# Optimization experiments

Measured on AMD Instinct MI355X. Metric: run time of the kernel, lower is better.

## Reference

```python
import jax, jax.numpy as jnp
import numpy as np

U_N, I_N, D, L, R = 50000, 25000, 64, 2, 2
E_UI, E_TR, E_II = 500000, 600000, 400000
B, K = 512, 100
EPS = 1e-8
LAMB = 0.5
L2_NORM = 1e-4


def setup_inputs() -> dict:
    key = jax.random.key(0)
    ks = jax.random.split(key, 16)
    f = lambda k, s: jax.random.normal(k, s, dtype=jnp.float32) * 0.05
    ri = lambda k, s, lo, hi: jax.random.randint(k, s, lo, hi, dtype=jnp.int32)
    return {
        "user_embedding": f(ks[0], (U_N, D)),
        "item_embedding": f(ks[1], (I_N, D)),
        "user_item_W": f(ks[2], (L, D, D)),
        "item_item_W": f(ks[3], (R, L, D, D)),
        "behavior_W": f(ks[4], (R, D * (L + 1), D * (L + 1))),
        "mgnn_weight": jax.random.normal(ks[5], (R,), dtype=jnp.float32),
        "rel_rows": ri(ks[6], (R, E_UI), 0, U_N),
        "rel_cols": ri(ks[7], (R, E_UI), 0, I_N),
        "train_rows": ri(ks[8], (E_TR,), 0, U_N),
        "train_cols": ri(ks[9], (E_TR,), 0, I_N),
        "ig_rows": ri(ks[10], (R, E_II), 0, I_N),
        "ig_cols": ri(ks[11], (R, E_II), 0, I_N),
        "user_behavior_degree": ri(ks[12], (U_N, R), 1, 50),
        "item_graph_degree": ri(ks[13], (R, I_N), 1, 50),
        "users": ri(ks[14], (B,), 0, U_N),
        "items": ri(ks[15], (B, K), 0, I_N),
    }


def _seg(data, seg_ids, n):
    return jax.ops.segment_sum(data, seg_ids, num_segments=n)


def _propagate(ue, ie, W_ui, W_ii, mgnn_weight,
               rel_rows, rel_cols, train_rows, train_cols,
               ig_rows, ig_cols, ubd, igd):
    Un, In = ue.shape[0], ie.shape[0]
    ubd_f = ubd.astype(jnp.float32)
    igd_f = igd.astype(jnp.float32)
    # per-user behavior mixing weights alpha_{u,t}
    w = jax.nn.softmax(mgnn_weight)                       # [R]
    total = ubd_f @ w[:, None]                            # [U,1]
    ubw = ubd_f * w[None, :] / (total + EPS)              # [U,R]
    # item degree from train matrix column sums (unit values)
    item_deg = _seg(jnp.ones((train_cols.shape[0],), jnp.float32), train_cols, In)[:, None] + EPS
    U_cur, I_cur = ue, ie
    U_list, I_list = [ue], [ie]
    S_lists = [[ie] for _ in range(R)]
    for l in range(L):
        # user <- item aggregation per behavior, weighted sum over behaviors
        U_neighbor = jnp.zeros_like(U_cur)
        for r in range(R):
            p = _seg(I_cur[rel_cols[r]], rel_rows[r], Un) / (ubd_f[:, r:r + 1] + EPS)
            U_neighbor = U_neighbor + ubw[:, r:r + 1] * p
        U_new = U_neighbor @ W_ui[l]
        # item <- user aggregation through train matrix transpose
        I_user = _seg(U_cur[train_rows], train_cols, In) / item_deg
        I_new = I_user @ W_ui[l]
        # item-item propagation per behavior
        for r in range(R):
            agg = _seg(I_cur[ig_cols[r]], ig_rows[r], In) / (igd_f[r][:, None] + EPS)
            S_lists[r].append(agg @ W_ii[r, l])
        U_cur, I_cur = U_new, I_new
        U_list.append(U_cur)
        I_list.append(I_cur)
    U_final = jnp.concatenate(U_list, axis=1)             # [U, D*(L+1)]
    I_final = jnp.concatenate(I_list, axis=1)             # [I, D*(L+1)]
    S_final = [jnp.concatenate(s, axis=1) for s in S_lists]
    return U_final, I_final, S_final


def reference(user_embedding, item_embedding, user_item_W, item_item_W,
              behavior_W, mgnn_weight, rel_rows, rel_cols, train_rows,
              train_cols, ig_rows, ig_cols, user_behavior_degree,
              item_graph_degree, users, items):
    Uf, If, Sf = _propagate(user_embedding, item_embedding, user_item_W,
                            item_item_W, mgnn_weight, rel_rows, rel_cols,
                            train_rows, train_cols, ig_rows, ig_cols,
                            user_behavior_degree, item_graph_degree)
    bu = Uf[users]                                        # [B, dt]
    bi = If[items]                                        # [B, K, dt]
    score1 = jnp.einsum('bd,bkd->bk', bu, bi)
    ubd_f = user_behavior_degree.astype(jnp.float32)
    Un = user_embedding.shape[0]
    score2 = jnp.zeros_like(score1)
    for r in range(R):
        s_emb = Sf[r]
        agg = _seg(s_emb[rel_cols[r]], rel_rows[r], Un) / (ubd_f[:, r:r + 1] + EPS)
        user_proj = agg @ behavior_W[r]                   # [U, dt]
        item_proj = s_emb @ behavior_W[r]                 # [I, dt]
        # gather-then-dot instead of full [B,I] matmul + gather (same math)
        score2 = score2 + jnp.einsum('bd,bkd->bk', user_proj[users], item_proj[items])
    score2 = score2 / R
    scores = LAMB * score1 + (1.0 - LAMB) * score2
    n_cand = items.shape[1]
    # original squares the [B,K,dt]-expanded user emb, hence the *K factor
    L2_loss = L2_NORM * (jnp.sum(bu ** 2) * n_cand + jnp.sum(bi ** 2))
    return scores, L2_loss
```

## Files before the change

kernel.cpp:

```cpp
#include <hip/hip_runtime.h>
#include <hip/hip_bf16.h>

#define U_NN   50000
#define I_NN   25000
#define DIM    64
#define EUI    500000
#define ETR    600000
#define EII    400000
#define NB     512
#define NK     100
#define EPSF   1e-8f
#define LAMBF  0.5f
#define L2NF   1e-4f
#define S_UI   48
#define S_TR   64
#define S_IG   48

typedef unsigned short bfu;

__device__ __forceinline__ bfu f2bf(float f) {
  unsigned int u = __float_as_uint(f);
  return (bfu)((u + 0x7fffu + ((u >> 16) & 1u)) >> 16);
}

__device__ __forceinline__ float4 bf4(uint2 p) {
  float4 r;
  r.x = __uint_as_float(p.x << 16);
  r.y = __uint_as_float(p.x & 0xffff0000u);
  r.z = __uint_as_float(p.y << 16);
  r.w = __uint_as_float(p.y & 0xffff0000u);
  return r;
}


__global__ void k_prep_user(const int* __restrict__ ubd, const float* __restrict__ mg,
                            float* __restrict__ scale1, float* __restrict__ scale2) {
  int u = blockIdx.x * 256 + threadIdx.x;
  if (u >= U_NN) return;
  float m0 = mg[0], m1 = mg[1];
  float mx = fmaxf(m0, m1);
  float e0 = expf(m0 - mx), e1 = expf(m1 - mx);
  float inv = 1.0f / (e0 + e1);
  float w0 = e0 * inv, w1 = e1 * inv;
  float d0 = (float)ubd[u * 2 + 0], d1 = (float)ubd[u * 2 + 1];
  float total = d0 * w0 + d1 * w1;
  float it = 1.0f / (total + EPSF);
  scale1[u * 2 + 0] = (d0 * w0 * it) / (d0 + EPSF);
  scale1[u * 2 + 1] = (d1 * w1 * it) / (d1 + EPSF);
  scale2[u * 2 + 0] = 1.0f / (d0 + EPSF);
  scale2[u * 2 + 1] = 1.0f / (d1 + EPSF);
}

__global__ void k_inv_int(const int* __restrict__ d, float* __restrict__ o, int n) {
  int i = blockIdx.x * 256 + threadIdx.x;
  if (i >= n) return;
  o[i] = 1.0f / ((float)d[i] + EPSF);
}

__global__ void k_transpose192(const float* __restrict__ BW, float* __restrict__ BWT) {
  int r = blockIdx.y;
  int i = blockIdx.x * 256 + threadIdx.x;
  if (i >= 192 * 192) return;
  int row = i / 192, col = i - row * 192;
  BWT[(size_t)r * 36864 + row * 192 + col] = BW[(size_t)r * 36864 + col * 192 + row];
}

__global__ void k_cvt(const float* __restrict__ s, bfu* __restrict__ d, int n4) {
  int i = blockIdx.x * 256 + threadIdx.x;
  if (i >= n4) return;
  float4 v = reinterpret_cast<const float4*>(s)[i];
  ushort4 o;
  o.x = f2bf(v.x); o.y = f2bf(v.y); o.z = f2bf(v.z); o.w = f2bf(v.w);
  reinterpret_cast<ushort4*>(d)[i] = o;
}


struct FillDesc { const int* key; const int* val; int n; int* cur; int* ec; int stride; int nk; };
struct FillDescs { FillDesc d[5]; };

__global__ void k_fill_r(FillDescs ds, int pass) {
  FillDesc sd = ds.d[blockIdx.y];
  int qk = sd.nk >> 2;
  int klo = qk * pass;
  int khi = (pass == 3) ? sd.nk : klo + qk;
  int base = blockIdx.x * 2048 + threadIdx.x;
  int kk[8], pp[8];
#pragma unroll
  for (int i = 0; i < 8; i++) {
    int e = base + i * 256;
    kk[i] = -1;
    if (e < sd.n) { int k = sd.key[e]; if (k >= klo && k < khi) kk[i] = k; }
  }
#pragma unroll
  for (int i = 0; i < 8; i++)
    pp[i] = (kk[i] >= 0) ? atomicAdd(&sd.cur[kk[i]], 1) : 0;
#pragma unroll
  for (int i = 0; i < 8; i++)
    if (kk[i] >= 0 && pp[i] < sd.stride)
      sd.ec[(size_t)kk[i] * sd.stride + pp[i]] = sd.val[base + i * 256];
}

struct AggDesc {
  const int* ecA; const int* curA; int strideA;
  const int* ecB; const int* curB; int strideB;
  const bfu* src;
  const float* W;
  float* out;
  bfu* outb;
  const float* sc;
  const int* map;
  int n;
  int mode;
};
struct AggDescs { AggDesc d[4]; };

__device__ __forceinline__ float4 wred(float4 a) {
  a.x += __shfl_xor(a.x, 16, 64); a.y += __shfl_xor(a.y, 16, 64);
  a.z += __shfl_xor(a.z, 16, 64); a.w += __shfl_xor(a.w, 16, 64);
  a.x += __shfl_xor(a.x, 32, 64); a.y += __shfl_xor(a.y, 32, 64);
  a.z += __shfl_xor(a.z, 32, 64); a.w += __shfl_xor(a.w, 32, 64);
  return a;
}

__device__ __forceinline__ float rdlane(float v, int l) {
  return __uint_as_float(__builtin_amdgcn_readlane(__float_as_uint(v), l));
}

#define ACC4(A, v) { A.x += v.x; A.y += v.y; A.z += v.z; A.w += v.w; }

__device__ __forceinline__ void gather4b(const int* __restrict__ l0, int d0,
                                         const int* __restrict__ l1, int d1,
                                         const int* __restrict__ l2, int d2,
                                         const int* __restrict__ l3, int d3,
                                         const bfu* __restrict__ src, int c4, int sub,
                                         float4& A0, float4& A1, float4& A2, float4& A3) {
  int j0 = sub, j1 = sub, j2 = sub, j3 = sub;
  while (j0 < d0 && j1 < d1 && j2 < d2 && j3 < d3) {
    uint2 p0 = *reinterpret_cast<const uint2*>(src + (size_t)l0[j0] * DIM + c4);
    uint2 p1 = *reinterpret_cast<const uint2*>(src + (size_t)l1[j1] * DIM + c4);
    uint2 p2 = *reinterpret_cast<const uint2*>(src + (size_t)l2[j2] * DIM + c4);
    uint2 p3 = *reinterpret_cast<const uint2*>(src + (size_t)l3[j3] * DIM + c4);
    float4 v0 = bf4(p0), v1 = bf4(p1), v2 = bf4(p2), v3 = bf4(p3);
    ACC4(A0, v0); ACC4(A1, v1); ACC4(A2, v2); ACC4(A3, v3);
    j0 += 4; j1 += 4; j2 += 4; j3 += 4;
  }
  for (; j0 < d0; j0 += 4) { float4 v = bf4(*reinterpret_cast<const uint2*>(src + (size_t)l0[j0] * DIM + c4)); ACC4(A0, v); }
  for (; j1 < d1; j1 += 4) { float4 v = bf4(*reinterpret_cast<const uint2*>(src + (size_t)l1[j1] * DIM + c4)); ACC4(A1, v); }
  for (; j2 < d2; j2 += 4) { float4 v = bf4(*reinterpret_cast<const uint2*>(src + (size_t)l2[j2] * DIM + c4)); ACC4(A2, v); }
  for (; j3 < d3; j3 += 4) { float4 v = bf4(*reinterpret_cast<const uint2*>(src + (size_t)l3[j3] * DIM + c4)); ACC4(A3, v); }
}

__device__ __forceinline__ void mm2(const float* wreg, float4 x0, float4 x1,
                                    float& y0, float& y1) {
  y0 = 0.f; y1 = 0.f;
#pragma unroll
  for (int sl = 0; sl < 16; sl++) {
    y0 = fmaf(rdlane(x0.x, sl), wreg[4 * sl + 0], y0);
    y0 = fmaf(rdlane(x0.y, sl), wreg[4 * sl + 1], y0);
    y0 = fmaf(rdlane(x0.z, sl), wreg[4 * sl + 2], y0);
    y0 = fmaf(rdlane(x0.w, sl), wreg[4 * sl + 3], y0);
    y1 = fmaf(rdlane(x1.x, sl), wreg[4 * sl + 0], y1);
    y1 = fmaf(rdlane(x1.y, sl), wreg[4 * sl + 1], y1);
    y1 = fmaf(rdlane(x1.z, sl), wreg[4 * sl + 2], y1);
    y1 = fmaf(rdlane(x1.w, sl), wreg[4 * sl + 3], y1);
  }
}

__device__ __forceinline__ float4 scale4(float4 a, float s) {
  float4 r; r.x = a.x * s; r.y = a.y * s; r.z = a.z * s; r.w = a.w * s; return r;
}

__global__ __launch_bounds__(256) void k_agg_mm(AggDescs ds) {
  AggDesc sd = ds.d[blockIdx.y];
  int rowBlk = blockIdx.x * 16;
  if (rowBlk >= sd.n) return;
  int t = threadIdx.x;
  int wv = t >> 6, lane = t & 63;
  int sub = lane >> 4, c4 = (lane & 15) * 4;
  float wreg[64];
#pragma unroll
  for (int k = 0; k < 64; k++) wreg[k] = sd.W[k * 64 + lane];
  int rowBase = rowBlk + wv * 4;

  if (sd.mode == 0) {
    for (int rep = 0; rep < 2; rep++) {
      int row0 = rowBase + rep * 2;
      int row1 = row0 + 1;
      if (row0 >= sd.n) break;
      bool ok1 = row1 < sd.n;
      int u0 = sd.map ? sd.map[row0] : row0;
      int u1 = ok1 ? (sd.map ? sd.map[row1] : row1) : u0;
      int dA0 = sd.curA[u0], dB0 = sd.curB[u0];
      int dA1 = ok1 ? sd.curA[u1] : 0;
      int dB1 = ok1 ? sd.curB[u1] : 0;
      const int* lA0 = sd.ecA + (size_t)u0 * sd.strideA;
      const int* lB0 = sd.ecB + (size_t)u0 * sd.strideB;
      const int* lA1 = sd.ecA + (size_t)u1 * sd.strideA;
      const int* lB1 = sd.ecB + (size_t)u1 * sd.strideB;
      float4 aA0 = {0,0,0,0}, aB0 = {0,0,0,0}, aA1 = {0,0,0,0}, aB1 = {0,0,0,0};
      gather4b(lA0, dA0, lB0, dB0, lA1, dA1, lB1, dB1, sd.src, c4, sub,
               aA0, aB0, aA1, aB1);
      aA0 = wred(aA0); aB0 = wred(aB0); aA1 = wred(aA1); aB1 = wred(aB1);
      float sA0 = sd.sc[u0 * 2], sB0 = sd.sc[u0 * 2 + 1];
      float sA1 = sd.sc[u1 * 2], sB1 = sd.sc[u1 * 2 + 1];
      float4 x0, x1;
      x0.x = sA0 * aA0.x + sB0 * aB0.x; x0.y = sA0 * aA0.y + sB0 * aB0.y;
      x0.z = sA0 * aA0.z + sB0 * aB0.z; x0.w = sA0 * aA0.w + sB0 * aB0.w;
      x1.x = sA1 * aA1.x + sB1 * aB1.x; x1.y = sA1 * aA1.y + sB1 * aB1.y;
      x1.z = sA1 * aA1.z + sB1 * aB1.z; x1.w = sA1 * aA1.w + sB1 * aB1.w;
      float y0, y1;
      mm2(wreg, x0, x1, y0, y1);
      sd.out[(size_t)row0 * DIM + lane] = y0;
      if (sd.outb) sd.outb[(size_t)row0 * DIM + lane] = f2bf(y0);
      if (ok1) {
        sd.out[(size_t)row1 * DIM + lane] = y1;
        if (sd.outb) sd.outb[(size_t)row1 * DIM + lane] = f2bf(y1);
      }
    }
  } else {
    int row0 = rowBase, row1 = rowBase + 1, row2 = rowBase + 2, row3 = rowBase + 3;
    if (row0 >= sd.n) return;
    bool ok1 = row1 < sd.n, ok2 = row2 < sd.n, ok3 = row3 < sd.n;
    int u1c = ok1 ? row1 : row0, u2c = ok2 ? row2 : row0, u3c = ok3 ? row3 : row0;
    int d0 = sd.curA[row0];
    int d1 = ok1 ? sd.curA[row1] : 0;
    int d2 = ok2 ? sd.curA[row2] : 0;
    int d3 = ok3 ? sd.curA[row3] : 0;
    const int* l0 = sd.ecA + (size_t)row0 * sd.strideA;
    const int* l1 = sd.ecA + (size_t)u1c * sd.strideA;
    const int* l2 = sd.ecA + (size_t)u2c * sd.strideA;
    const int* l3 = sd.ecA + (size_t)u3c * sd.strideA;
    float4 a0 = {0,0,0,0}, a1 = {0,0,0,0}, a2 = {0,0,0,0}, a3 = {0,0,0,0};
    gather4b(l0, d0, l1, d1, l2, d2, l3, d3, sd.src, c4, sub, a0, a1, a2, a3);
    a0 = wred(a0); a1 = wred(a1); a2 = wred(a2); a3 = wred(a3);
    float s0, s1, s2, s3;
    if (sd.mode == 1) {
      s0 = 1.0f / ((float)d0 + EPSF); s1 = 1.0f / ((float)d1 + EPSF);
      s2 = 1.0f / ((float)d2 + EPSF); s3 = 1.0f / ((float)d3 + EPSF);
    } else {
      s0 = sd.sc[row0]; s1 = ok1 ? sd.sc[row1] : 0.f;
      s2 = ok2 ? sd.sc[row2] : 0.f; s3 = ok3 ? sd.sc[row3] : 0.f;
    }
    float4 x0 = scale4(a0, s0), x1 = scale4(a1, s1);
    float4 x2 = scale4(a2, s2), x3 = scale4(a3, s3);
    float y0, y1, y2, y3;
    mm2(wreg, x0, x1, y0, y1);
    mm2(wreg, x2, x3, y2, y3);
    sd.out[(size_t)row0 * DIM + lane] = y0;
    if (sd.outb) sd.outb[(size_t)row0 * DIM + lane] = f2bf(y0);
    if (ok1) { sd.out[(size_t)row1 * DIM + lane] = y1;
               if (sd.outb) sd.outb[(size_t)row1 * DIM + lane] = f2bf(y1); }
    if (ok2) { sd.out[(size_t)row2 * DIM + lane] = y2;
               if (sd.outb) sd.outb[(size_t)row2 * DIM + lane] = f2bf(y2); }
    if (ok3) { sd.out[(size_t)row3 * DIM + lane] = y3;
               if (sd.outb) sd.outb[(size_t)row3 * DIM + lane] = f2bf(y3); }
  }
}

__global__ void k_agg_score(const int* __restrict__ ec0, const int* __restrict__ cur0,
                            const int* __restrict__ ec1, const int* __restrict__ cur1,
                            const int* __restrict__ users, const float* __restrict__ scale2,
                            const bfu* __restrict__ I0b,
                            const bfu* __restrict__ S0ab, const bfu* __restrict__ S0bb,
                            const bfu* __restrict__ S1ab, const bfu* __restrict__ S1bb,
                            float* __restrict__ aggB) {
  int b = blockIdx.x, r = blockIdx.y;
  int w = threadIdx.x >> 6, lane = threadIdx.x & 63;
  int sub = lane >> 4, c4 = (lane & 15) * 4;
  int u = users[b];
  const int* ec = (r ? ec1 : ec0) + (size_t)u * S_UI;
  int d = (r ? cur1 : cur0)[u];
  const bfu* src = (w == 0) ? I0b : (w == 1) ? (r ? S1ab : S0ab) : (r ? S1bb : S0bb);
  float4 acc = {0.f, 0.f, 0.f, 0.f};
  for (int j = sub; j < d; j += 4) {
    float4 v = bf4(*reinterpret_cast<const uint2*>(src + (size_t)ec[j] * DIM + c4));
    acc.x += v.x; acc.y += v.y; acc.z += v.z; acc.w += v.w;
  }
  acc = wred(acc);
  if (sub == 0) {
    float s = scale2[u * 2 + r];
    float4 o = { acc.x * s, acc.y * s, acc.z * s, acc.w * s };
    *reinterpret_cast<float4*>(aggB + ((size_t)r * NB + b) * 192 + w * 64 + c4) = o;
  }
}


struct M192Desc { const float* X0; const float* X1; const float* X2; int xStride;
                  const float* W; float* Y; int n; };
struct M192Descs { M192Desc d[2]; };

__global__ void k_matmul192(M192Descs ds) {
  M192Desc sd = ds.d[blockIdx.y];
  int r0 = blockIdx.x * 64;
  if (r0 >= sd.n) return;
  __shared__ float Wl[32 * 192];
  __shared__ float xs[64][32];
  int t = threadIdx.x;
  int rg = t >> 6, col = t & 63;
  float acc[16][3];
#pragma unroll
  for (int j = 0; j < 16; j++) { acc[j][0] = 0.f; acc[j][1] = 0.f; acc[j][2] = 0.f; }
  for (int kc = 0; kc < 6; kc++) {
    const float* Xc = (kc < 2) ? sd.X0 : ((kc < 4) ? sd.X1 : sd.X2);
    int xoff = (kc & 1) * 32;
#pragma unroll
    for (int tt = 0; tt < 8; tt++) {
      int e = t + tt * 256;
      int rr = e >> 5, cc = e & 31;
      int row = r0 + rr;
      xs[rr][cc] = (row < sd.n) ? Xc[(size_t)row * sd.xStride + xoff + cc] : 0.0f;
    }
#pragma unroll
    for (int tt = 0; tt < 24; tt++) {
      int e = t + tt * 256;
      Wl[e] = sd.W[(size_t)(kc * 32) * 192 + e];
    }
    __syncthreads();
    for (int k = 0; k < 32; k++) {
      float w0 = Wl[k * 192 + col];
      float w1 = Wl[k * 192 + 64 + col];
      float w2 = Wl[k * 192 + 128 + col];
#pragma unroll
      for (int j = 0; j < 16; j++) {
        float x = xs[rg * 16 + j][k];
        acc[j][0] += x * w0; acc[j][1] += x * w1; acc[j][2] += x * w2;
      }
    }
    __syncthreads();
  }
  for (int j = 0; j < 16; j++) {
    int row = r0 + rg * 16 + j;
    if (row < sd.n) {
      sd.Y[(size_t)row * 192 + col]       = acc[j][0];
      sd.Y[(size_t)row * 192 + 64 + col]  = acc[j][1];
      sd.Y[(size_t)row * 192 + 128 + col] = acc[j][2];
    }
  }
}

__global__ void k_score_all(const int* __restrict__ users, const int* __restrict__ items,
                            const float* __restrict__ U0, const float* __restrict__ U1,
                            const float* __restrict__ U2B,
                            const float* __restrict__ I0, const float* __restrict__ I1,
                            const float* __restrict__ I2,
                            const float* __restrict__ S0a, const float* __restrict__ S0b,
                            const float* __restrict__ S1a, const float* __restrict__ S1b,
                            const float* __restrict__ upB2,
                            float* __restrict__ out) {
  int b = blockIdx.x, t = threadIdx.x;
  int wave = t >> 6, lane = t & 63;
  int u = users[b];
  float uf0 = U0[(size_t)u * 64 + lane];
  float uf1 = U1[(size_t)u * 64 + lane];
  float uf2 = U2B[(size_t)b * 64 + lane];
  const float* u20 = upB2 + (size_t)b * 192;
  const float* u21 = upB2 + (size_t)(NB + b) * 192;
  float av0 = u20[lane] + u21[lane];
  float a01 = u20[64 + lane], a02 = u20[128 + lane];
  float a11 = u21[64 + lane], a12 = u21[128 + lane];
  float l2acc = (wave == 0) ? (uf0 * uf0 + uf1 * uf1 + uf2 * uf2) * (float)NK : 0.0f;
  for (int k = wave * 25; k < wave * 25 + 25; k++) {
    int it = items[b * NK + k];
    float v0  = I0[(size_t)it * 64 + lane];
    float v1  = I1[(size_t)it * 64 + lane];
    float v2  = I2[(size_t)it * 64 + lane];
    float w0a = S0a[(size_t)it * 64 + lane];
    float w0b = S0b[(size_t)it * 64 + lane];
    float w1a = S1a[(size_t)it * 64 + lane];
    float w1b = S1b[(size_t)it * 64 + lane];
    float p = LAMBF * (uf0 * v0 + uf1 * v1 + uf2 * v2)
            + 0.25f * (av0 * v0 + a01 * w0a + a02 * w0b + a11 * w1a + a12 * w1b);
    l2acc += v0 * v0 + v1 * v1 + v2 * v2;
#pragma unroll
    for (int m = 1; m < 64; m <<= 1) p += __shfl_xor(p, m, 64);
    if (lane == 0) out[b * NK + k] = p;
  }
#pragma unroll
  for (int m = 1; m < 64; m <<= 1) l2acc += __shfl_xor(l2acc, m, 64);
  __shared__ float ws4[4];
  if (lane == 0) ws4[wave] = l2acc;
  __syncthreads();
  if (t == 0) atomicAdd(out + NB * NK, (ws4[0] + ws4[1] + ws4[2] + ws4[3]) * L2NF);
}


extern "C" void kernel_launch(void* const* d_in, const int* in_sizes, int n_in,
                              void* d_out, int out_size, void* d_ws, size_t ws_size,
                              hipStream_t stream) {
  const float* U0  = (const float*)d_in[0];
  const float* I0  = (const float*)d_in[1];
  const float* Wui = (const float*)d_in[2];
  const float* Wii = (const float*)d_in[3];
  const float* BW  = (const float*)d_in[4];
  const float* mg  = (const float*)d_in[5];
  const int* rel_rows   = (const int*)d_in[6];
  const int* rel_cols   = (const int*)d_in[7];
  const int* train_rows = (const int*)d_in[8];
  const int* train_cols = (const int*)d_in[9];
  const int* ig_rows    = (const int*)d_in[10];
  const int* ig_cols    = (const int*)d_in[11];
  const int* ubd        = (const int*)d_in[12];
  const int* igd        = (const int*)d_in[13];
  const int* users      = (const int*)d_in[14];
  const int* items      = (const int*)d_in[15];
  float* out = (float*)d_out;

  char* wptr = (char*)d_ws;
  auto alloci = [&](size_t n) -> int* {
    int* p = (int*)wptr;
    wptr += ((n * 4 + 255) / 256) * 256;
    return p;
  };
  auto allocf = [&](size_t n) -> float* { return (float*)alloci(n); };
  auto allocb = [&](size_t n) -> bfu* {
    bfu* p = (bfu*)wptr;
    wptr += ((n * 2 + 255) / 256) * 256;
    return p;
  };

  float* scale1 = allocf((size_t)U_NN * 2);
  float* scale2 = allocf((size_t)U_NN * 2);
  float* invig  = allocf((size_t)2 * I_NN);
  float* BWT    = allocf((size_t)2 * 192 * 192);
  int* c0  = alloci(U_NN);
  int* c1  = alloci(U_NN);
  int* cT  = alloci(I_NN);
  int* cG0 = alloci(I_NN);
  int* cG1 = alloci(I_NN);
  size_t curBytes = (size_t)(wptr - (char*)c0);
  int* ec0  = alloci((size_t)U_NN * S_UI);
  int* ec1  = alloci((size_t)U_NN * S_UI);
  int* ecT  = alloci((size_t)I_NN * S_TR);
  int* ecG0 = alloci((size_t)I_NN * S_IG);
  int* ecG1 = alloci((size_t)I_NN * S_IG);
  float* U1  = allocf((size_t)U_NN * 64);
  float* I1  = allocf((size_t)I_NN * 64);
  float* I2  = allocf((size_t)I_NN * 64);
  float* S0a = allocf((size_t)I_NN * 64);
  float* S0b = allocf((size_t)I_NN * 64);
  float* S1a = allocf((size_t)I_NN * 64);
  float* S1b = allocf((size_t)I_NN * 64);
  float* U2B = allocf((size_t)NB * 64);
  float* aggB = allocf((size_t)2 * NB * 192);
  float* upBt = allocf((size_t)2 * NB * 192);
  float* upB2 = allocf((size_t)2 * NB * 192);
  bfu* U0b  = allocb((size_t)U_NN * 64);
  bfu* I0b  = allocb((size_t)I_NN * 64);
  bfu* U1b  = allocb((size_t)U_NN * 64);
  bfu* I1b  = allocb((size_t)I_NN * 64);
  bfu* S0ab = allocb((size_t)I_NN * 64);
  bfu* S0bb = allocb((size_t)I_NN * 64);
  bfu* S1ab = allocb((size_t)I_NN * 64);
  bfu* S1bb = allocb((size_t)I_NN * 64);

  const int gU = (U_NN + 255) / 256;
  const int gI2 = (2 * I_NN + 255) / 256;

  hipMemsetAsync(c0, 0, curBytes, stream);
  k_prep_user<<<gU, 256, 0, stream>>>(ubd, mg, scale1, scale2);
  k_inv_int<<<gI2, 256, 0, stream>>>(igd, invig, 2 * I_NN);
  k_transpose192<<<dim3(144, 2), 256, 0, stream>>>(BW, BWT);
  k_cvt<<<(U_NN * 16 + 255) / 256, 256, 0, stream>>>(U0, U0b, U_NN * 16);
  k_cvt<<<(I_NN * 16 + 255) / 256, 256, 0, stream>>>(I0, I0b, I_NN * 16);

  FillDescs fd;
  fd.d[0] = { rel_rows,       rel_cols,       EUI, c0,  ec0,  S_UI, U_NN };
  fd.d[1] = { rel_rows + EUI, rel_cols + EUI, EUI, c1,  ec1,  S_UI, U_NN };
  fd.d[2] = { train_cols,     train_rows,     ETR, cT,  ecT,  S_TR, I_NN };
  fd.d[3] = { ig_rows,        ig_cols,        EII, cG0, ecG0, S_IG, I_NN };
  fd.d[4] = { ig_rows + EII,  ig_cols + EII,  EII, cG1, ecG1, S_IG, I_NN };
  const int gE8 = (ETR + 2047) / 2048;
  for (int p = 0; p < 4; p++)
    k_fill_r<<<dim3(gE8, 5), 256, 0, stream>>>(fd, p);

  AggDescs a0;
  a0.d[0] = { ec0, c0, S_UI, ec1, c1, S_UI, I0b, Wui,            U1,  U1b,  scale1, nullptr, U_NN, 0 };
  a0.d[1] = { ecT, cT, S_TR, nullptr, nullptr, 0, U0b, Wui,      I1,  I1b,  nullptr, nullptr, I_NN, 1 };
  a0.d[2] = { ecG0, cG0, S_IG, nullptr, nullptr, 0, I0b, Wii + 0 * 4096, S0a, S0ab, invig,        nullptr, I_NN, 2 };
  a0.d[3] = { ecG1, cG1, S_IG, nullptr, nullptr, 0, I0b, Wii + 2 * 4096, S1a, S1ab, invig + I_NN, nullptr, I_NN, 2 };
  k_agg_mm<<<dim3((U_NN + 15) / 16, 4), 256, 0, stream>>>(a0);

  AggDescs a1;
  a1.d[0] = { ec0, c0, S_UI, ec1, c1, S_UI, I1b, Wui + 4096,     U2B, nullptr, scale1, users,  NB,   0 };
  a1.d[1] = { ecT, cT, S_TR, nullptr, nullptr, 0, U1b, Wui + 4096, I2, nullptr, nullptr, nullptr, I_NN, 1 };
  a1.d[2] = { ecG0, cG0, S_IG, nullptr, nullptr, 0, I1b, Wii + 1 * 4096, S0b, S0bb, invig,        nullptr, I_NN, 2 };
  a1.d[3] = { ecG1, cG1, S_IG, nullptr, nullptr, 0, I1b, Wii + 3 * 4096, S1b, S1bb, invig + I_NN, nullptr, I_NN, 2 };
  k_agg_mm<<<dim3((I_NN + 15) / 16, 4), 256, 0, stream>>>(a1);

  k_agg_score<<<dim3(NB, 2), 192, 0, stream>>>(ec0, c0, ec1, c1, users, scale2,
                                               I0b, S0ab, S0bb, S1ab, S1bb, aggB);
  M192Descs mU;
  mU.d[0] = { aggB,            aggB + 64,            aggB + 128,            192, BW,         upBt,            NB };
  mU.d[1] = { aggB + NB * 192, aggB + NB * 192 + 64, aggB + NB * 192 + 128, 192, BW + 36864, upBt + NB * 192, NB };
  k_matmul192<<<dim3((NB + 63) / 64, 2), 256, 0, stream>>>(mU);
  M192Descs mU2;
  mU2.d[0] = { upBt,            upBt + 64,            upBt + 128,            192, BWT,         upB2,            NB };
  mU2.d[1] = { upBt + NB * 192, upBt + NB * 192 + 64, upBt + NB * 192 + 128, 192, BWT + 36864, upB2 + NB * 192, NB };
  k_matmul192<<<dim3((NB + 63) / 64, 2), 256, 0, stream>>>(mU2);

  hipMemsetAsync(out + (size_t)NB * NK, 0, 4, stream);
  k_score_all<<<NB, 256, 0, stream>>>(users, items, U0, U1, U2B,
                                      I0, I1, I2, S0a, S0b, S1a, S1b, upB2, out);
}
```

Before: 619.3 us.

## Transform-then-aggregate: precompute X@W in bf16 before neighbor gather

Reorders each propagation layer so node features are first multiplied by the 64x64 weight in a separate dense kernel that writes bf16, then the gather-aggregate kernel only sums the pre-transformed rows and scales them. This relies on linearity, (sum x)W = sum(xW). It removes the readlane-based matmul and the 64-register weight load from the latency-bound gather kernel. The gather loop is also rewritten as predicated, max-degree-bounded iterations with two edges per step, and results are written as vectorized float4. In exchange it adds two extra kernel launches and extra memory traffic for eight transformed tables, and rounding now happens after the transform rather than before.

```diff
diff --git a/kernel.cpp b/kernel.cpp
--- a/kernel.cpp
+++ b/kernel.cpp
@@ -100,19 +100,6 @@
       sd.ec[(size_t)kk[i] * sd.stride + pp[i]] = sd.val[base + i * 256];
 }
 
-struct AggDesc {
-  const int* ecA; const int* curA; int strideA;
-  const int* ecB; const int* curB; int strideB;
-  const bfu* src;
-  const float* W;
-  float* out;
-  bfu* outb;
-  const float* sc;
-  const int* map;
-  int n;
-  int mode;
-};
-struct AggDescs { AggDesc d[4]; };
 
 __device__ __forceinline__ float4 wred(float4 a) {
   a.x += __shfl_xor(a.x, 16, 64); a.y += __shfl_xor(a.y, 16, 64);
@@ -126,28 +113,20 @@
   return __uint_as_float(__builtin_amdgcn_readlane(__float_as_uint(v), l));
 }
 
-#define ACC4(A, v) { A.x += v.x; A.y += v.y; A.z += v.z; A.w += v.w; }
-
-__device__ __forceinline__ void gather4b(const int* __restrict__ l0, int d0,
-                                         const int* __restrict__ l1, int d1,
-                                         const int* __restrict__ l2, int d2,
-                                         const int* __restrict__ l3, int d3,
-                                         const bfu* __restrict__ src, int c4, int sub,
-                                         float4& A0, float4& A1, float4& A2, float4& A3) {
-  int j0 = sub, j1 = sub, j2 = sub, j3 = sub;
-  while (j0 < d0 && j1 < d1 && j2 < d2 && j3 < d3) {
-    uint2 p0 = *reinterpret_cast<const uint2*>(src + (size_t)l0[j0] * DIM + c4);
-    uint2 p1 = *reinterpret_cast<const uint2*>(src + (size_t)l1[j1] * DIM + c4);
-    uint2 p2 = *reinterpret_cast<const uint2*>(src + (size_t)l2[j2] * DIM + c4);
-    uint2 p3 = *reinterpret_cast<const uint2*>(src + (size_t)l3[j3] * DIM + c4);
-    float4 v0 = bf4(p0), v1 = bf4(p1), v2 = bf4(p2), v3 = bf4(p3);
-    ACC4(A0, v0); ACC4(A1, v1); ACC4(A2, v2); ACC4(A3, v3);
-    j0 += 4; j1 += 4; j2 += 4; j3 += 4;
-  }
-  for (; j0 < d0; j0 += 4) { float4 v = bf4(*reinterpret_cast<const uint2*>(src + (size_t)l0[j0] * DIM + c4)); ACC4(A0, v); }
-  for (; j1 < d1; j1 += 4) { float4 v = bf4(*reinterpret_cast<const uint2*>(src + (size_t)l1[j1] * DIM + c4)); ACC4(A1, v); }
-  for (; j2 < d2; j2 += 4) { float4 v = bf4(*reinterpret_cast<const uint2*>(src + (size_t)l2[j2] * DIM + c4)); ACC4(A2, v); }
-  for (; j3 < d3; j3 += 4) { float4 v = bf4(*reinterpret_cast<const uint2*>(src + (size_t)l3[j3] * DIM + c4)); ACC4(A3, v); }
+__device__ __forceinline__ float4 scale4(float4 a, float s) {
+  float4 r; r.x = a.x * s; r.y = a.y * s; r.z = a.z * s; r.w = a.w * s; return r;
+}
+
+__device__ __forceinline__ void medge(const int* __restrict__ l, int j, int d,
+                                      const bfu* __restrict__ src, int c4, float4& A) {
+  int jj = (j < d) ? j : 0;
+  int idx = l[jj];
+  idx = (j < d) ? idx : 0;
+  uint2 p = *reinterpret_cast<const uint2*>(src + (size_t)idx * DIM + c4);
+  if (j < d) {
+    float4 v = bf4(p);
+    A.x += v.x; A.y += v.y; A.z += v.z; A.w += v.w;
+  }
 }
 
 __device__ __forceinline__ void mm2(const float* wreg, float4 x0, float4 x1,
@@ -166,21 +145,55 @@
   }
 }
 
-__device__ __forceinline__ float4 scale4(float4 a, float s) {
-  float4 r; r.x = a.x * s; r.y = a.y * s; r.z = a.z * s; r.w = a.w * s; return r;
-}
-
-__global__ __launch_bounds__(256) void k_agg_mm(AggDescs ds) {
+struct TDesc { const float* src; const float* W; bfu* outb; int n; };
+struct TDescs { TDesc d[4]; };
+
+__global__ __launch_bounds__(256) void k_mm64t(TDescs ds) {
+  TDesc sd = ds.d[blockIdx.y];
+  int rowBase = blockIdx.x * 16 + (threadIdx.x >> 6) * 4;
+  if (rowBase >= sd.n) return;
+  int lane = threadIdx.x & 63;
+  int c4 = (lane & 15) * 4;
+  float wreg[64];
+#pragma unroll
+  for (int k = 0; k < 64; k++) wreg[k] = sd.W[k * 64 + lane];
+  int r0 = rowBase, r1 = rowBase + 1, r2 = rowBase + 2, r3 = rowBase + 3;
+  bool ok1 = r1 < sd.n, ok2 = r2 < sd.n, ok3 = r3 < sd.n;
+  float4 x0 = *reinterpret_cast<const float4*>(sd.src + (size_t)r0 * 64 + c4);
+  float4 x1 = ok1 ? *reinterpret_cast<const float4*>(sd.src + (size_t)r1 * 64 + c4) : x0;
+  float4 x2 = ok2 ? *reinterpret_cast<const float4*>(sd.src + (size_t)r2 * 64 + c4) : x0;
+  float4 x3 = ok3 ? *reinterpret_cast<const float4*>(sd.src + (size_t)r3 * 64 + c4) : x0;
+  float y0, y1, y2, y3;
+  mm2(wreg, x0, x1, y0, y1);
+  mm2(wreg, x2, x3, y2, y3);
+  sd.outb[(size_t)r0 * 64 + lane] = f2bf(y0);
+  if (ok1) sd.outb[(size_t)r1 * 64 + lane] = f2bf(y1);
+  if (ok2) sd.outb[(size_t)r2 * 64 + lane] = f2bf(y2);
+  if (ok3) sd.outb[(size_t)r3 * 64 + lane] = f2bf(y3);
+}
+
+struct AggDesc {
+  const int* ecA; const int* curA; int strideA;
+  const int* ecB; const int* curB; int strideB;
+  const bfu* src;
+  float* out;
+  bfu* outb;
+  const float* sc;
+  const int* map;
+  int n;
+  int mode;
+};
+struct AggDescs { AggDesc d[4]; };
+
+__global__ __launch_bounds__(256) void k_agg(AggDescs ds) {
   AggDesc sd = ds.d[blockIdx.y];
   int rowBlk = blockIdx.x * 16;
   if (rowBlk >= sd.n) return;
   int t = threadIdx.x;
   int wv = t >> 6, lane = t & 63;
   int sub = lane >> 4, c4 = (lane & 15) * 4;
-  float wreg[64];
-#pragma unroll
-  for (int k = 0; k < 64; k++) wreg[k] = sd.W[k * 64 + lane];
   int rowBase = rowBlk + wv * 4;
+  if (rowBase >= sd.n) return;
 
   if (sd.mode == 0) {
     for (int rep = 0; rep < 2; rep++) {
@@ -197,63 +210,75 @@
       const int* lB0 = sd.ecB + (size_t)u0 * sd.strideB;
       const int* lA1 = sd.ecA + (size_t)u1 * sd.strideA;
       const int* lB1 = sd.ecB + (size_t)u1 * sd.strideB;
-      float4 aA0 = {0,0,0,0}, aB0 = {0,0,0,0}, aA1 = {0,0,0,0}, aB1 = {0,0,0,0};
-      gather4b(lA0, dA0, lB0, dB0, lA1, dA1, lB1, dB1, sd.src, c4, sub,
-               aA0, aB0, aA1, aB1);
-      aA0 = wred(aA0); aB0 = wred(aB0); aA1 = wred(aA1); aB1 = wred(aB1);
+      int maxd = max(max(dA0, dB0), max(dA1, dB1));
+      float4 A0 = {0,0,0,0}, B0 = {0,0,0,0}, A1 = {0,0,0,0}, B1 = {0,0,0,0};
+      for (int j = sub; j < maxd; j += 8) {
+        medge(lA0, j, dA0, sd.src, c4, A0);
+        medge(lB0, j, dB0, sd.src, c4, B0);
+        medge(lA1, j, dA1, sd.src, c4, A1);
+        medge(lB1, j, dB1, sd.src, c4, B1);
+        medge(lA0, j + 4, dA0, sd.src, c4, A0);
+        medge(lB0, j + 4, dB0, sd.src, c4, B0);
+        medge(lA1, j + 4, dA1, sd.src, c4, A1);
+        medge(lB1, j + 4, dB1, sd.src, c4, B1);
+      }
+      A0 = wred(A0); B0 = wred(B0); A1 = wred(A1); B1 = wred(B1);
       float sA0 = sd.sc[u0 * 2], sB0 = sd.sc[u0 * 2 + 1];
       float sA1 = sd.sc[u1 * 2], sB1 = sd.sc[u1 * 2 + 1];
       float4 x0, x1;
-      x0.x = sA0 * aA0.x + sB0 * aB0.x; x0.y = sA0 * aA0.y + sB0 * aB0.y;
-      x0.z = sA0 * aA0.z + sB0 * aB0.z; x0.w = sA0 * aA0.w + sB0 * aB0.w;
-      x1.x = sA1 * aA1.x + sB1 * aB1.x; x1.y = sA1 * aA1.y + sB1 * aB1.y;
-      x1.z = sA1 * aA1.z + sB1 * aB1.z; x1.w = sA1 * aA1.w + sB1 * aB1.w;
-      float y0, y1;
-      mm2(wreg, x0, x1, y0, y1);
-      sd.out[(size_t)row0 * DIM + lane] = y0;
-      if (sd.outb) sd.outb[(size_t)row0 * DIM + lane] = f2bf(y0);
-      if (ok1) {
-        sd.out[(size_t)row1 * DIM + lane] = y1;
-        if (sd.outb) sd.outb[(size_t)row1 * DIM + lane] = f2bf(y1);
-      }
+      x0.x = sA0 * A0.x + sB0 * B0.x; x0.y = sA0 * A0.y + sB0 * B0.y;
+      x0.z = sA0 * A0.z + sB0 * B0.z; x0.w = sA0 * A0.w + sB0 * B0.w;
+      x1.x = sA1 * A1.x + sB1 * B1.x; x1.y = sA1 * A1.y + sB1 * B1.y;
+      x1.z = sA1 * A1.z + sB1 * B1.z; x1.w = sA1 * A1.w + sB1 * B1.w;
+      float4 o = (sub == 0) ? x0 : x1;
+      int row = row0 + sub;
+      if (sub < 2 && row < sd.n)
+        *reinterpret_cast<float4*>(sd.out + (size_t)row * DIM + c4) = o;
     }
   } else {
-    int row0 = rowBase, row1 = rowBase + 1, row2 = rowBase + 2, row3 = rowBase + 3;
-    if (row0 >= sd.n) return;
-    bool ok1 = row1 < sd.n, ok2 = row2 < sd.n, ok3 = row3 < sd.n;
-    int u1c = ok1 ? row1 : row0, u2c = ok2 ? row2 : row0, u3c = ok3 ? row3 : row0;
-    int d0 = sd.curA[row0];
-    int d1 = ok1 ? sd.curA[row1] : 0;
-    int d2 = ok2 ? sd.curA[row2] : 0;
-    int d3 = ok3 ? sd.curA[row3] : 0;
-    const int* l0 = sd.ecA + (size_t)row0 * sd.strideA;
+    int r0 = rowBase, r1 = rowBase + 1, r2 = rowBase + 2, r3 = rowBase + 3;
+    bool ok1 = r1 < sd.n, ok2 = r2 < sd.n, ok3 = r3 < sd.n;
+    int u1c = ok1 ? r1 : r0, u2c = ok2 ? r2 : r0, u3c = ok3 ? r3 : r0;
+    int d0 = sd.curA[r0];
+    int d1 = ok1 ? sd.curA[r1] : 0;
+    int d2 = ok2 ? sd.curA[r2] : 0;
+    int d3 = ok3 ? sd.curA[r3] : 0;
+    const int* l0 = sd.ecA + (size_t)r0 * sd.strideA;
     const int* l1 = sd.ecA + (size_t)u1c * sd.strideA;
     const int* l2 = sd.ecA + (size_t)u2c * sd.strideA;
     const int* l3 = sd.ecA + (size_t)u3c * sd.strideA;
-    float4 a0 = {0,0,0,0}, a1 = {0,0,0,0}, a2 = {0,0,0,0}, a3 = {0,0,0,0};
-    gather4b(l0, d0, l1, d1, l2, d2, l3, d3, sd.src, c4, sub, a0, a1, a2, a3);
-    a0 = wred(a0); a1 = wred(a1); a2 = wred(a2); a3 = wred(a3);
+    int maxd = max(max(d0, d1), max(d2, d3));
+    float4 A0 = {0,0,0,0}, A1 = {0,0,0,0}, A2 = {0,0,0,0}, A3 = {0,0,0,0};
+    for (int j = sub; j < maxd; j += 8) {
+      medge(l0, j, d0, sd.src, c4, A0);
+      medge(l1, j, d1, sd.src, c4, A1);
+      medge(l2, j, d2, sd.src, c4, A2);
+      medge(l3, j, d3, sd.src, c4, A3);
+      medge(l0, j + 4, d0, sd.src, c4, A0);
+      medge(l1, j + 4, d1, sd.src, c4, A1);
+      medge(l2, j + 4, d2, sd.src, c4, A2);
+      medge(l3, j + 4, d3, sd.src, c4, A3);
+    }
+    A0 = wred(A0); A1 = wred(A1); A2 = wred(A2); A3 = wred(A3);
     float s0, s1, s2, s3;
     if (sd.mode == 1) {
       s0 = 1.0f / ((float)d0 + EPSF); s1 = 1.0f / ((float)d1 + EPSF);
       s2 = 1.0f / ((float)d2 + EPSF); s3 = 1.0f / ((float)d3 + EPSF);
     } else {
-      s0 = sd.sc[row0]; s1 = ok1 ? sd.sc[row1] : 0.f;
-      s2 = ok2 ? sd.sc[row2] : 0.f; s3 = ok3 ? sd.sc[row3] : 0.f;
-    }
-    float4 x0 = scale4(a0, s0), x1 = scale4(a1, s1);
-    float4 x2 = scale4(a2, s2), x3 = scale4(a3, s3);
-    float y0, y1, y2, y3;
-    mm2(wreg, x0, x1, y0, y1);
-    mm2(wreg, x2, x3, y2, y3);
-    sd.out[(size_t)row0 * DIM + lane] = y0;
-    if (sd.outb) sd.outb[(size_t)row0 * DIM + lane] = f2bf(y0);
-    if (ok1) { sd.out[(size_t)row1 * DIM + lane] = y1;
-               if (sd.outb) sd.outb[(size_t)row1 * DIM + lane] = f2bf(y1); }
-    if (ok2) { sd.out[(size_t)row2 * DIM + lane] = y2;
-               if (sd.outb) sd.outb[(size_t)row2 * DIM + lane] = f2bf(y2); }
-    if (ok3) { sd.out[(size_t)row3 * DIM + lane] = y3;
-               if (sd.outb) sd.outb[(size_t)row3 * DIM + lane] = f2bf(y3); }
+      s0 = sd.sc[r0]; s1 = ok1 ? sd.sc[r1] : 0.f;
+      s2 = ok2 ? sd.sc[r2] : 0.f; s3 = ok3 ? sd.sc[r3] : 0.f;
+    }
+    float4 o = (sub == 0) ? A0 : (sub == 1) ? A1 : (sub == 2) ? A2 : A3;
+    float ss = (sub == 0) ? s0 : (sub == 1) ? s1 : (sub == 2) ? s2 : s3;
+    int row = rowBase + sub;
+    if (row < sd.n) {
+      o = scale4(o, ss);
+      *reinterpret_cast<float4*>(sd.out + (size_t)row * DIM + c4) = o;
+      if (sd.outb) {
+        ushort4 ob = { f2bf(o.x), f2bf(o.y), f2bf(o.z), f2bf(o.w) };
+        *reinterpret_cast<ushort4*>(sd.outb + (size_t)row * DIM + c4) = ob;
+      }
+    }
   }
 }
 
@@ -444,23 +469,29 @@
   float* aggB = allocf((size_t)2 * NB * 192);
   float* upBt = allocf((size_t)2 * NB * 192);
   float* upB2 = allocf((size_t)2 * NB * 192);
-  bfu* U0b  = allocb((size_t)U_NN * 64);
   bfu* I0b  = allocb((size_t)I_NN * 64);
-  bfu* U1b  = allocb((size_t)U_NN * 64);
-  bfu* I1b  = allocb((size_t)I_NN * 64);
   bfu* S0ab = allocb((size_t)I_NN * 64);
   bfu* S0bb = allocb((size_t)I_NN * 64);
   bfu* S1ab = allocb((size_t)I_NN * 64);
   bfu* S1bb = allocb((size_t)I_NN * 64);
+  bfu* T_I0ui  = allocb((size_t)I_NN * 64);
+  bfu* T_U0ui  = allocb((size_t)U_NN * 64);
+  bfu* T_I0ii0 = allocb((size_t)I_NN * 64);
+  bfu* T_I0ii1 = allocb((size_t)I_NN * 64);
+  bfu* T_I1ui  = allocb((size_t)I_NN * 64);
+  bfu* T_U1ui  = allocb((size_t)U_NN * 64);
+  bfu* T_I1ii0 = allocb((size_t)I_NN * 64);
+  bfu* T_I1ii1 = allocb((size_t)I_NN * 64);
 
   const int gU = (U_NN + 255) / 256;
   const int gI2 = (2 * I_NN + 255) / 256;
+  const int gT = (U_NN + 15) / 16;
+  const int gTI = (I_NN + 15) / 16;
 
   hipMemsetAsync(c0, 0, curBytes, stream);
   k_prep_user<<<gU, 256, 0, stream>>>(ubd, mg, scale1, scale2);
   k_inv_int<<<gI2, 256, 0, stream>>>(igd, invig, 2 * I_NN);
   k_transpose192<<<dim3(144, 2), 256, 0, stream>>>(BW, BWT);
-  k_cvt<<<(U_NN * 16 + 255) / 256, 256, 0, stream>>>(U0, U0b, U_NN * 16);
   k_cvt<<<(I_NN * 16 + 255) / 256, 256, 0, stream>>>(I0, I0b, I_NN * 16);
 
   FillDescs fd;
@@ -473,19 +504,33 @@
   for (int p = 0; p < 4; p++)
     k_fill_r<<<dim3(gE8, 5), 256, 0, stream>>>(fd, p);
 
+  TDescs t0;
+  t0.d[0] = { I0, Wui,            T_I0ui,  I_NN };
+  t0.d[1] = { U0, Wui,            T_U0ui,  U_NN };
+  t0.d[2] = { I0, Wii + 0 * 4096, T_I0ii0, I_NN };
+  t0.d[3] = { I0, Wii + 2 * 4096, T_I0ii1, I_NN };
+  k_mm64t<<<dim3(gT, 4), 256, 0, stream>>>(t0);
+
   AggDescs a0;
-  a0.d[0] = { ec0, c0, S_UI, ec1, c1, S_UI, I0b, Wui,            U1,  U1b,  scale1, nullptr, U_NN, 0 };
-  a0.d[1] = { ecT, cT, S_TR, nullptr, nullptr, 0, U0b, Wui,      I1,  I1b,  nullptr, nullptr, I_NN, 1 };
-  a0.d[2] = { ecG0, cG0, S_IG, nullptr, nullptr, 0, I0b, Wii + 0 * 4096, S0a, S0ab, invig,        nullptr, I_NN, 2 };
-  a0.d[3] = { ecG1, cG1, S_IG, nullptr, nullptr, 0, I0b, Wii + 2 * 4096, S1a, S1ab, invig + I_NN, nullptr, I_NN, 2 };
-  k_agg_mm<<<dim3((U_NN + 15) / 16, 4), 256, 0, stream>>>(a0);
+  a0.d[0] = { ec0, c0, S_UI, ec1, c1, S_UI, T_I0ui,  U1,  nullptr, scale1, nullptr, U_NN, 0 };
+  a0.d[1] = { ecT, cT, S_TR, nullptr, nullptr, 0, T_U0ui,  I1,  nullptr, nullptr, nullptr, I_NN, 1 };
+  a0.d[2] = { ecG0, cG0, S_IG, nullptr, nullptr, 0, T_I0ii0, S0a, S0ab, invig,        nullptr, I_NN, 2 };
+  a0.d[3] = { ecG1, cG1, S_IG, nullptr, nullptr, 0, T_I0ii1, S1a, S1ab, invig + I_NN, nullptr, I_NN, 2 };
+  k_agg<<<dim3(gT, 4), 256, 0, stream>>>(a0);
+
+  TDescs t1;
+  t1.d[0] = { I1, Wui + 4096,     T_I1ui,  I_NN };
+  t1.d[1] = { U1, Wui + 4096,     T_U1ui,  U_NN };
+  t1.d[2] = { I1, Wii + 1 * 4096, T_I1ii0, I_NN };
+  t1.d[3] = { I1, Wii + 3 * 4096, T_I1ii1, I_NN };
+  k_mm64t<<<dim3(gT, 4), 256, 0, stream>>>(t1);
 
   AggDescs a1;
-  a1.d[0] = { ec0, c0, S_UI, ec1, c1, S_UI, I1b, Wui + 4096,     U2B, nullptr, scale1, users,  NB,   0 };
-  a1.d[1] = { ecT, cT, S_TR, nullptr, nullptr, 0, U1b, Wui + 4096, I2, nullptr, nullptr, nullptr, I_NN, 1 };
-  a1.d[2] = { ecG0, cG0, S_IG, nullptr, nullptr, 0, I1b, Wii + 1 * 4096, S0b, S0bb, invig,        nullptr, I_NN, 2 };
-  a1.d[3] = { ecG1, cG1, S_IG, nullptr, nullptr, 0, I1b, Wii + 3 * 4096, S1b, S1bb, invig + I_NN, nullptr, I_NN, 2 };
-  k_agg_mm<<<dim3((I_NN + 15) / 16, 4), 256, 0, stream>>>(a1);
+  a1.d[0] = { ec0, c0, S_UI, ec1, c1, S_UI, T_I1ui,  U2B, nullptr, scale1, users,  NB,   0 };
+  a1.d[1] = { ecT, cT, S_TR, nullptr, nullptr, 0, T_U1ui,  I2,  nullptr, nullptr, nullptr, I_NN, 1 };
+  a1.d[2] = { ecG0, cG0, S_IG, nullptr, nullptr, 0, T_I1ii0, S0b, S0bb, invig,        nullptr, I_NN, 2 };
+  a1.d[3] = { ecG1, cG1, S_IG, nullptr, nullptr, 0, T_I1ii1, S1b, S1bb, invig + I_NN, nullptr, I_NN, 2 };
+  k_agg<<<dim3(gTI, 4), 256, 0, stream>>>(a1);
 
   k_agg_score<<<dim3(NB, 2), 192, 0, stream>>>(ec0, c0, ec1, c1, users, scale2,
                                                I0b, S0ab, S0bb, S1ab, S1bb, aggB);
```

After: 669.5 us. 1.08x slower.
